# Kernel optimization log

Hardware: AMD Instinct MI355X
Metric: run time of the kernel (lower is better)

## Reference

```python
import jax, jax.numpy as jnp
import numpy as np

N_NODES = 100000
N_EDGES = 1600000
D_IN = 128
D_OUT = 128
EPS = 1e-5


def setup_inputs() -> dict:
    key = jax.random.key(0)
    ks = jax.random.split(key, 5)
    x = jax.random.normal(ks[0], (N_NODES, D_IN), dtype=jnp.float32)
    edge_index = jax.random.randint(ks[1], (2, N_EDGES), 0, N_NODES, dtype=jnp.int64)
    scale = 1.0 / np.sqrt(D_IN)
    W_root = jax.random.normal(ks[2], (D_IN, D_OUT), dtype=jnp.float32) * scale
    W_rel = jax.random.normal(ks[3], (D_IN, D_OUT), dtype=jnp.float32) * scale
    b_rel = jax.random.normal(ks[4], (D_OUT,), dtype=jnp.float32) * 0.01
    gamma = jnp.ones((D_OUT,), dtype=jnp.float32)
    beta = jnp.zeros((D_OUT,), dtype=jnp.float32)
    return {"x": x, "edge_index": edge_index, "W_root": W_root, "W_rel": W_rel,
            "b_rel": b_rel, "gamma": gamma, "beta": beta}


def reference(x, edge_index, W_root, W_rel, b_rel, gamma, beta):
    # GraphConv: out = aggr(x_j) @ W_rel + b_rel + x @ W_root   (aggr = sum)
    src = edge_index[0]
    dst = edge_index[1]
    aggr = jax.ops.segment_sum(x[src], dst, num_segments=x.shape[0])  # [N, D_IN]
    h = aggr @ W_rel + b_rel + x @ W_root                              # [N, D_OUT]
    # NodeLevelBatchNorm (training mode: batch stats over node dim, biased var)
    mean = jnp.mean(h, axis=0)
    var = jnp.mean(jnp.square(h - mean), axis=0)
    h_norm = (h - mean) * jax.lax.rsqrt(var + EPS) * gamma + beta
    return jax.nn.relu(h_norm)
```

## Files before the change

kernel.cpp:

```cpp
#include <hip/hip_runtime.h>

#define N_NODES 100000
#define N_EDGES 1600000
#define D 128
#define NB 196
#define EPT 10
#define CHUNK 2560
#define BIN_BLOCKS 625
#define CVT_X_BLOCKS 6250
#define ZROW N_NODES
#define PBK 13312

typedef __bf16 bf16x8 __attribute__((ext_vector_type(8)));
typedef float f32x4 __attribute__((ext_vector_type(4)));

__device__ __forceinline__ unsigned f2bf(float f) {
    unsigned u = __float_as_uint(f);
    return (u + 0x7fffu + ((u >> 16) & 1u)) >> 16;
}
__device__ __forceinline__ float bf_lo(unsigned u) { return __uint_as_float(u << 16); }
__device__ __forceinline__ float bf_hi(unsigned u) { return __uint_as_float(u & 0xffff0000u); }

__global__ __launch_bounds__(256) void prep_kernel(const float* __restrict__ x,
                                                   const float* __restrict__ Wrel,
                                                   const float* __restrict__ Wroot,
                                                   const int* __restrict__ ei,
                                                   unsigned short* __restrict__ x_bf,
                                                   unsigned short* __restrict__ Wt,
                                                   int* __restrict__ bcount) {
    __shared__ int h[256];
    int b = blockIdx.x;
    int t = threadIdx.x;
    if (b < CVT_X_BLOCKS) {
        size_t i = ((size_t)b * 256 + t) * 8;
        float4 v0 = *(const float4*)(x + i);
        float4 v1 = *(const float4*)(x + i + 4);
        uint4 p;
        p.x = f2bf(v0.x) | (f2bf(v0.y) << 16);
        p.y = f2bf(v0.z) | (f2bf(v0.w) << 16);
        p.z = f2bf(v1.x) | (f2bf(v1.y) << 16);
        p.w = f2bf(v1.z) | (f2bf(v1.w) << 16);
        *(uint4*)(x_bf + i) = p;
    } else if (b < CVT_X_BLOCKS + 128) {
        int c = b - CVT_X_BLOCKS;
        float v = (t < 128) ? Wrel[t * D + c] : Wroot[(t - 128) * D + c];
        Wt[c * 256 + t] = (unsigned short)f2bf(v);
    } else if (b == CVT_X_BLOCKS + 128) {
        if (t < 16) *(uint4*)(x_bf + (size_t)ZROW * D + t * 8) = make_uint4(0, 0, 0, 0);
    } else {
        int blk = b - (CVT_X_BLOCKS + 129);
        h[t] = 0;
        __syncthreads();
        int base = blk * CHUNK;
#pragma unroll
        for (int i = 0; i < EPT; ++i) {
            int dst = ei[N_EDGES + base + i * 256 + t];
            atomicAdd(&h[dst >> 9], 1);
        }
        __syncthreads();
        if (t < NB && h[t]) atomicAdd(&bcount[t], h[t]);
    }
}

__global__ __launch_bounds__(256) void bscan_kernel(const int* __restrict__ bcount,
                                                    int* __restrict__ bucket_base,
                                                    int* __restrict__ bcur) {
    __shared__ int s[256];
    int t = threadIdx.x;
    int v = (t < NB) ? bcount[t] : 0;
    s[t] = v;
    __syncthreads();
    for (int off = 1; off < 256; off <<= 1) {
        int a = (t >= off) ? s[t - off] : 0;
        __syncthreads();
        s[t] += a;
        __syncthreads();
    }
    int excl = s[t] - v;
    if (t < NB) {
        bucket_base[t] = excl;
        bcur[t] = excl;
    }
    if (t == NB) bucket_base[NB] = N_EDGES;
}

__global__ __launch_bounds__(256) void binify_kernel(const int* __restrict__ ei,
                                                     int* __restrict__ bcur,
                                                     unsigned* __restrict__ epk) {
    __shared__ int lhist[256];
    __shared__ int lstart[256];
    __shared__ int lfill[256];
    __shared__ int gbase[256];
    __shared__ uint2 stage[CHUNK];

    int t = threadIdx.x;
    int base = blockIdx.x * CHUNK;
    lhist[t] = 0;
    lfill[t] = 0;
    __syncthreads();

    int src[EPT], dst[EPT];
#pragma unroll
    for (int i = 0; i < EPT; ++i) {
        int e = base + i * 256 + t;
        src[i] = ei[e];
        dst[i] = ei[N_EDGES + e];
        atomicAdd(&lhist[dst[i] >> 9], 1);
    }
    __syncthreads();

    int v = lhist[t];
    lstart[t] = v;
    __syncthreads();
    for (int off = 1; off < 256; off <<= 1) {
        int a = (t >= off) ? lstart[t - off] : 0;
        __syncthreads();
        lstart[t] += a;
        __syncthreads();
    }
    int excl = lstart[t] - v;
    if (t < NB && v > 0) gbase[t] = atomicAdd(&bcur[t], v);
    __syncthreads();
    lstart[t] = excl;
    __syncthreads();

#pragma unroll
    for (int i = 0; i < EPT; ++i) {
        int b = dst[i] >> 9;
        int lp = atomicAdd(&lfill[b], 1);
        stage[lstart[b] + lp] = make_uint2((unsigned)src[i], (unsigned)dst[i]);
    }
    __syncthreads();

    for (int i = t; i < CHUNK; i += 256) {
        uint2 p = stage[i];
        int b = (int)(p.y >> 9);
        unsigned code = p.x | ((p.y & 511u) << 17);
        epk[gbase[b] + (i - lstart[b])] = code;
    }
}

__global__ __launch_bounds__(256) void place_kernel(const unsigned* __restrict__ epk,
                                                    const int* __restrict__ bucket_base,
                                                    int* __restrict__ rbeg,
                                                    int* __restrict__ rend,
                                                    int* __restrict__ srcs) {
    __shared__ int cnt[512];
    __shared__ int sA[512];
    __shared__ int sB[512];
    __shared__ int cursor[512];
    int b = blockIdx.x;
    int t = threadIdx.x;
    int pbeg = bucket_base[b];
    int pend = bucket_base[b + 1];
    int R = b * PBK;

    cnt[t] = 0;
    cnt[t + 256] = 0;
    __syncthreads();
    for (int i = pbeg + t; i < pend; i += 256)
        atomicAdd(&cnt[epk[i] >> 17], 1);
    __syncthreads();

    for (int j = t; j < 512; j += 256) sA[j] = j ? ((cnt[j - 1] + 7) & ~7) : 0;
    __syncthreads();
    int* cur = sA;
    int* nxt = sB;
    for (int off = 1; off < 512; off <<= 1) {
        for (int j = t; j < 512; j += 256)
            nxt[j] = cur[j] + ((j >= off) ? cur[j - off] : 0);
        __syncthreads();
        int* tm = cur; cur = nxt; nxt = tm;
    }

    for (int j = t; j < 512; j += 256) {
        int pj = (cnt[j] + 7) & ~7;
        int s = R + cur[j];
        int g = (b << 9) + j;
        if (g < 100352) { rbeg[g] = s; rend[g] = s + pj; }
        cursor[j] = s;
    }
    __syncthreads();

    for (int i = pbeg + t; i < pend; i += 256) {
        unsigned code = epk[i];
        int pos = atomicAdd(&cursor[code >> 17], 1);
        srcs[pos] = (int)(code & 0x1FFFFu);
    }
    __syncthreads();

    for (int j = t; j < 512; j += 256) {
        int endp = R + cur[j] + ((cnt[j] + 7) & ~7);
        for (int p = cursor[j]; p < endp; ++p) srcs[p] = ZROW;
    }
}

__global__ __launch_bounds__(256) void gather_kernel(const unsigned short* __restrict__ x_bf,
                                                     const int* __restrict__ rbeg,
                                                     const int* __restrict__ rend,
                                                     const int* __restrict__ srcs,
                                                     unsigned short* __restrict__ aggr_bf) {
    int t = threadIdx.x;
    int node = blockIdx.x * 16 + (t >> 4);
    int l16 = t & 15;
    int e = rbeg[node];
    int end = rend[node];
    const unsigned short* xp = x_bf + l16 * 8;
    float a0 = 0.f, a1 = 0.f, a2 = 0.f, a3 = 0.f;
    float a4 = 0.f, a5 = 0.f, a6 = 0.f, a7 = 0.f;
    for (; e + 15 < end; e += 16) {
        int4 s0 = *(const int4*)(srcs + e);
        int4 s1 = *(const int4*)(srcs + e + 4);
        int4 s2 = *(const int4*)(srcs + e + 8);
        int4 s3 = *(const int4*)(srcs + e + 12);
        uint4 u[16];
        u[0]  = *(const uint4*)(xp + (size_t)s0.x * D);
        u[1]  = *(const uint4*)(xp + (size_t)s0.y * D);
        u[2]  = *(const uint4*)(xp + (size_t)s0.z * D);
        u[3]  = *(const uint4*)(xp + (size_t)s0.w * D);
        u[4]  = *(const uint4*)(xp + (size_t)s1.x * D);
        u[5]  = *(const uint4*)(xp + (size_t)s1.y * D);
        u[6]  = *(const uint4*)(xp + (size_t)s1.z * D);
        u[7]  = *(const uint4*)(xp + (size_t)s1.w * D);
        u[8]  = *(const uint4*)(xp + (size_t)s2.x * D);
        u[9]  = *(const uint4*)(xp + (size_t)s2.y * D);
        u[10] = *(const uint4*)(xp + (size_t)s2.z * D);
        u[11] = *(const uint4*)(xp + (size_t)s2.w * D);
        u[12] = *(const uint4*)(xp + (size_t)s3.x * D);
        u[13] = *(const uint4*)(xp + (size_t)s3.y * D);
        u[14] = *(const uint4*)(xp + (size_t)s3.z * D);
        u[15] = *(const uint4*)(xp + (size_t)s3.w * D);
#pragma unroll
        for (int i = 0; i < 16; ++i) {
            a0 += bf_lo(u[i].x);
            a1 += bf_hi(u[i].x);
            a2 += bf_lo(u[i].y);
            a3 += bf_hi(u[i].y);
            a4 += bf_lo(u[i].z);
            a5 += bf_hi(u[i].z);
            a6 += bf_lo(u[i].w);
            a7 += bf_hi(u[i].w);
        }
    }
    if (e < end) {
        int4 s0 = *(const int4*)(srcs + e);
        int4 s1 = *(const int4*)(srcs + e + 4);
        uint4 u[8];
        u[0] = *(const uint4*)(xp + (size_t)s0.x * D);
        u[1] = *(const uint4*)(xp + (size_t)s0.y * D);
        u[2] = *(const uint4*)(xp + (size_t)s0.z * D);
        u[3] = *(const uint4*)(xp + (size_t)s0.w * D);
        u[4] = *(const uint4*)(xp + (size_t)s1.x * D);
        u[5] = *(const uint4*)(xp + (size_t)s1.y * D);
        u[6] = *(const uint4*)(xp + (size_t)s1.z * D);
        u[7] = *(const uint4*)(xp + (size_t)s1.w * D);
#pragma unroll
        for (int i = 0; i < 8; ++i) {
            a0 += bf_lo(u[i].x);
            a1 += bf_hi(u[i].x);
            a2 += bf_lo(u[i].y);
            a3 += bf_hi(u[i].y);
            a4 += bf_lo(u[i].z);
            a5 += bf_hi(u[i].z);
            a6 += bf_lo(u[i].w);
            a7 += bf_hi(u[i].w);
        }
    }
    uint4 w;
    w.x = f2bf(a0) | (f2bf(a1) << 16);
    w.y = f2bf(a2) | (f2bf(a3) << 16);
    w.z = f2bf(a4) | (f2bf(a5) << 16);
    w.w = f2bf(a6) | (f2bf(a7) << 16);
    *(uint4*)(aggr_bf + (size_t)node * D + l16 * 8) = w;
}

__global__ __launch_bounds__(256) void gemm_mfma(const unsigned short* __restrict__ aggr_bf,
                                                 const unsigned short* __restrict__ x_bf,
                                                 const unsigned short* __restrict__ Wt,
                                                 const float* __restrict__ brel,
                                                 unsigned short* __restrict__ h_bf,
                                                 float* __restrict__ gsum,
                                                 float* __restrict__ gss) {
    __shared__ unsigned short Bf[2048 * 8];
    __shared__ float sbias[128];
    __shared__ float SredS[4][128];
    __shared__ float SredQ[4][128];

    const int t = threadIdx.x;
    const int wave = t >> 6;
    const int lane = t & 63;
    const int quad = lane >> 4;
    const int l16 = lane & 15;
    const int blockRow = blockIdx.x * 128;

    if (t < 128) sbias[t] = brel[t];

    f32x4 acc[2][8];
#pragma unroll
    for (int i = 0; i < 2; ++i)
#pragma unroll
        for (int j = 0; j < 8; ++j) acc[i][j] = (f32x4){0.f, 0.f, 0.f, 0.f};

    const int rowb = blockRow + wave * 32;

#pragma unroll
    for (int half = 0; half < 2; ++half) {
#pragma unroll
        for (int f = t; f < 2048; f += 256) {
            int kcl = f >> 9;
            int ct = (f >> 6) & 7;
            int ln = f & 63;
            int col = ct * 16 + (ln & 15);
            int kb = half * 128 + kcl * 32 + ((ln >> 4) << 3);
            *(uint4*)&Bf[f * 8] = *(const uint4*)(Wt + col * 256 + kb);
        }
        __syncthreads();

        const unsigned short* Asrc = half ? x_bf : aggr_bf;
#pragma unroll
        for (int kcl = 0; kcl < 4; ++kcl) {
            const int k0 = kcl * 32 + quad * 8;
            bf16x8 af0 = *(const bf16x8*)(Asrc + (size_t)(rowb + l16) * D + k0);
            bf16x8 af1 = *(const bf16x8*)(Asrc + (size_t)(rowb + 16 + l16) * D + k0);
#pragma unroll
            for (int ct = 0; ct < 8; ++ct) {
                bf16x8 bfrag = *(const bf16x8*)&Bf[((kcl * 8 + ct) * 64 + lane) * 8];
                acc[0][ct] = __builtin_amdgcn_mfma_f32_16x16x32_bf16(af0, bfrag, acc[0][ct], 0, 0, 0);
                acc[1][ct] = __builtin_amdgcn_mfma_f32_16x16x32_bf16(af1, bfrag, acc[1][ct], 0, 0, 0);
            }
        }
        if (half == 0) __syncthreads();
    }

    float csum[8], css[8];
#pragma unroll
    for (int ct = 0; ct < 8; ++ct) { csum[ct] = 0.f; css[ct] = 0.f; }

#pragma unroll
    for (int rt = 0; rt < 2; ++rt) {
#pragma unroll
        for (int ct = 0; ct < 8; ++ct) {
            int col = ct * 16 + l16;
            float bv = sbias[col];
#pragma unroll
            for (int reg = 0; reg < 4; ++reg) {
                int row = blockRow + wave * 32 + rt * 16 + quad * 4 + reg;
                if (row < N_NODES) {
                    float v = acc[rt][ct][reg] + bv;
                    h_bf[(size_t)row * D + col] = (unsigned short)f2bf(v);
                    csum[ct] += v;
                    css[ct] += v * v;
                }
            }
        }
    }
#pragma unroll
    for (int ct = 0; ct < 8; ++ct) {
        float s = csum[ct], q = css[ct];
        s += __shfl_xor(s, 16);
        s += __shfl_xor(s, 32);
        q += __shfl_xor(q, 16);
        q += __shfl_xor(q, 32);
        if (quad == 0) {
            SredS[wave][ct * 16 + l16] = s;
            SredQ[wave][ct * 16 + l16] = q;
        }
    }
    __syncthreads();
    if (t < 128) {
        float s = SredS[0][t] + SredS[1][t] + SredS[2][t] + SredS[3][t];
        float q = SredQ[0][t] + SredQ[1][t] + SredQ[2][t] + SredQ[3][t];
        unsafeAtomicAdd(&gsum[t], s);
        unsafeAtomicAdd(&gss[t], q);
    }
}

__global__ __launch_bounds__(256) void norm_kernel(const unsigned short* __restrict__ h_bf,
                                                   float* __restrict__ out,
                                                   const float* __restrict__ gsum,
                                                   const float* __restrict__ gss,
                                                   const float* __restrict__ gamma,
                                                   const float* __restrict__ beta) {
    __shared__ float sscale[128];
    __shared__ float sshift[128];
    int t = threadIdx.x;
    if (t < 128) {
        const float inv_n = 1.0f / (float)N_NODES;
        float mean = gsum[t] * inv_n;
        float var = gss[t] * inv_n - mean * mean;
        float rs = rsqrtf(var + 1e-5f);
        float sc = gamma[t] * rs;
        sscale[t] = sc;
        sshift[t] = beta[t] - mean * sc;
    }
    __syncthreads();
    size_t e = ((size_t)blockIdx.x * 256 + t) * 4;
    if (e >= (size_t)N_NODES * D) return;
    int c = (int)(e & 127);
    uint2 u = *(const uint2*)(h_bf + e);
    float4 v;
    v.x = fmaxf(bf_lo(u.x) * sscale[c + 0] + sshift[c + 0], 0.f);
    v.y = fmaxf(bf_hi(u.x) * sscale[c + 1] + sshift[c + 1], 0.f);
    v.z = fmaxf(bf_lo(u.y) * sscale[c + 2] + sshift[c + 2], 0.f);
    v.w = fmaxf(bf_hi(u.y) * sscale[c + 3] + sshift[c + 3], 0.f);
    *(float4*)(out + e) = v;
}

extern "C" void kernel_launch(void* const* d_in, const int* in_sizes, int n_in,
                              void* d_out, int out_size, void* d_ws, size_t ws_size,
                              hipStream_t stream) {
    const float* x     = (const float*)d_in[0];
    const int*   ei    = (const int*)d_in[1];
    const float* Wroot = (const float*)d_in[2];
    const float* Wrel  = (const float*)d_in[3];
    const float* brel  = (const float*)d_in[4];
    const float* gamma = (const float*)d_in[5];
    const float* beta  = (const float*)d_in[6];
    float* out = (float*)d_out;

    unsigned short* aggr_bf = (unsigned short*)d_ws;
    unsigned short* x_bf    = aggr_bf + (size_t)N_NODES * D;
    unsigned short* Wt      = x_bf + (size_t)(N_NODES + 1) * D;
    float* gsum  = (float*)(Wt + 128 * 256);
    float* gss   = gsum + 128;
    int* bcount  = (int*)(gss + 128);
    int* bucket_base = bcount + 256;
    int* bcur    = bucket_base + 256;
    int* rbeg    = bcur + 256;
    int* rend    = rbeg + 100352;
    unsigned* epk = (unsigned*)(rend + 100352);
    int* srcs    = (int*)(epk + N_EDGES);
    unsigned short* h_bf = (unsigned short*)epk;

    hipMemsetAsync(gsum, 0, 512 * sizeof(int), stream);

    prep_kernel<<<CVT_X_BLOCKS + 129 + BIN_BLOCKS, 256, 0, stream>>>(
        x, Wrel, Wroot, ei, x_bf, Wt, bcount);
    bscan_kernel<<<1, 256, 0, stream>>>(bcount, bucket_base, bcur);
    binify_kernel<<<BIN_BLOCKS, 256, 0, stream>>>(ei, bcur, epk);
    place_kernel<<<NB, 256, 0, stream>>>(epk, bucket_base, rbeg, rend, srcs);
    gather_kernel<<<N_NODES / 16, 256, 0, stream>>>(x_bf, rbeg, rend, srcs, aggr_bf);
    gemm_mfma<<<(N_NODES + 127) / 128, 256, 0, stream>>>(aggr_bf, x_bf, Wt, brel, h_bf, gsum, gss);
    norm_kernel<<<12500, 256, 0, stream>>>(h_bf, out, gsum, gss, gamma, beta);
}
```

Before: 287.7 us.

## Fuse neighbor gather into MFMA GEMM via shared-memory A tile

Replaces the separate gather kernel and GEMM with one kernel. Each block gathers aggregated features for its 128 rows directly into an LDS tile laid out in MFMA fragment order, then runs both GEMM halves. This removes the global write and re-read of the bf16 aggregate buffer and one launch. In exchange, LDS use per block doubles, which lowers occupancy for the latency-bound gather, and the gather loop has fewer loads in flight per thread.

```diff
diff --git a/kernel.cpp b/kernel.cpp
--- a/kernel.cpp
+++ b/kernel.cpp
@@ -195,92 +195,16 @@
     }
 }
 
-__global__ __launch_bounds__(256) void gather_kernel(const unsigned short* __restrict__ x_bf,
-                                                     const int* __restrict__ rbeg,
-                                                     const int* __restrict__ rend,
-                                                     const int* __restrict__ srcs,
-                                                     unsigned short* __restrict__ aggr_bf) {
-    int t = threadIdx.x;
-    int node = blockIdx.x * 16 + (t >> 4);
-    int l16 = t & 15;
-    int e = rbeg[node];
-    int end = rend[node];
-    const unsigned short* xp = x_bf + l16 * 8;
-    float a0 = 0.f, a1 = 0.f, a2 = 0.f, a3 = 0.f;
-    float a4 = 0.f, a5 = 0.f, a6 = 0.f, a7 = 0.f;
-    for (; e + 15 < end; e += 16) {
-        int4 s0 = *(const int4*)(srcs + e);
-        int4 s1 = *(const int4*)(srcs + e + 4);
-        int4 s2 = *(const int4*)(srcs + e + 8);
-        int4 s3 = *(const int4*)(srcs + e + 12);
-        uint4 u[16];
-        u[0]  = *(const uint4*)(xp + (size_t)s0.x * D);
-        u[1]  = *(const uint4*)(xp + (size_t)s0.y * D);
-        u[2]  = *(const uint4*)(xp + (size_t)s0.z * D);
-        u[3]  = *(const uint4*)(xp + (size_t)s0.w * D);
-        u[4]  = *(const uint4*)(xp + (size_t)s1.x * D);
-        u[5]  = *(const uint4*)(xp + (size_t)s1.y * D);
-        u[6]  = *(const uint4*)(xp + (size_t)s1.z * D);
-        u[7]  = *(const uint4*)(xp + (size_t)s1.w * D);
-        u[8]  = *(const uint4*)(xp + (size_t)s2.x * D);
-        u[9]  = *(const uint4*)(xp + (size_t)s2.y * D);
-        u[10] = *(const uint4*)(xp + (size_t)s2.z * D);
-        u[11] = *(const uint4*)(xp + (size_t)s2.w * D);
-        u[12] = *(const uint4*)(xp + (size_t)s3.x * D);
-        u[13] = *(const uint4*)(xp + (size_t)s3.y * D);
-        u[14] = *(const uint4*)(xp + (size_t)s3.z * D);
-        u[15] = *(const uint4*)(xp + (size_t)s3.w * D);
-#pragma unroll
-        for (int i = 0; i < 16; ++i) {
-            a0 += bf_lo(u[i].x);
-            a1 += bf_hi(u[i].x);
-            a2 += bf_lo(u[i].y);
-            a3 += bf_hi(u[i].y);
-            a4 += bf_lo(u[i].z);
-            a5 += bf_hi(u[i].z);
-            a6 += bf_lo(u[i].w);
-            a7 += bf_hi(u[i].w);
-        }
-    }
-    if (e < end) {
-        int4 s0 = *(const int4*)(srcs + e);
-        int4 s1 = *(const int4*)(srcs + e + 4);
-        uint4 u[8];
-        u[0] = *(const uint4*)(xp + (size_t)s0.x * D);
-        u[1] = *(const uint4*)(xp + (size_t)s0.y * D);
-        u[2] = *(const uint4*)(xp + (size_t)s0.z * D);
-        u[3] = *(const uint4*)(xp + (size_t)s0.w * D);
-        u[4] = *(const uint4*)(xp + (size_t)s1.x * D);
-        u[5] = *(const uint4*)(xp + (size_t)s1.y * D);
-        u[6] = *(const uint4*)(xp + (size_t)s1.z * D);
-        u[7] = *(const uint4*)(xp + (size_t)s1.w * D);
-#pragma unroll
-        for (int i = 0; i < 8; ++i) {
-            a0 += bf_lo(u[i].x);
-            a1 += bf_hi(u[i].x);
-            a2 += bf_lo(u[i].y);
-            a3 += bf_hi(u[i].y);
-            a4 += bf_lo(u[i].z);
-            a5 += bf_hi(u[i].z);
-            a6 += bf_lo(u[i].w);
-            a7 += bf_hi(u[i].w);
-        }
-    }
-    uint4 w;
-    w.x = f2bf(a0) | (f2bf(a1) << 16);
-    w.y = f2bf(a2) | (f2bf(a3) << 16);
-    w.z = f2bf(a4) | (f2bf(a5) << 16);
-    w.w = f2bf(a6) | (f2bf(a7) << 16);
-    *(uint4*)(aggr_bf + (size_t)node * D + l16 * 8) = w;
-}
-
-__global__ __launch_bounds__(256) void gemm_mfma(const unsigned short* __restrict__ aggr_bf,
-                                                 const unsigned short* __restrict__ x_bf,
-                                                 const unsigned short* __restrict__ Wt,
-                                                 const float* __restrict__ brel,
-                                                 unsigned short* __restrict__ h_bf,
-                                                 float* __restrict__ gsum,
-                                                 float* __restrict__ gss) {
+__global__ __launch_bounds__(256) void fused_gemm(const unsigned short* __restrict__ x_bf,
+                                                  const int* __restrict__ rbeg,
+                                                  const int* __restrict__ rend,
+                                                  const int* __restrict__ srcs,
+                                                  const unsigned short* __restrict__ Wt,
+                                                  const float* __restrict__ brel,
+                                                  unsigned short* __restrict__ h_bf,
+                                                  float* __restrict__ gsum,
+                                                  float* __restrict__ gss) {
+    __shared__ unsigned short Af[2048 * 8];
     __shared__ unsigned short Bf[2048 * 8];
     __shared__ float sbias[128];
     __shared__ float SredS[4][128];
@@ -295,41 +219,107 @@
 
     if (t < 128) sbias[t] = brel[t];
 
+#pragma unroll
+    for (int f = t; f < 2048; f += 256) {
+        int kcl = f >> 9;
+        int ct = (f >> 6) & 7;
+        int ln = f & 63;
+        int col = ct * 16 + (ln & 15);
+        int kb = kcl * 32 + ((ln >> 4) << 3);
+        *(uint4*)&Bf[f * 8] = *(const uint4*)(Wt + col * 256 + kb);
+    }
+
+    const unsigned short* xp = x_bf + l16 * 8;
+#pragma unroll 1
+    for (int g = 0; g < 8; ++g) {
+        int r = wave * 32 + g * 4 + quad;
+        int node = blockRow + r;
+        int e = rbeg[node];
+        int end = rend[node];
+        float a0 = 0.f, a1 = 0.f, a2 = 0.f, a3 = 0.f;
+        float a4 = 0.f, a5 = 0.f, a6 = 0.f, a7 = 0.f;
+        for (; e < end; e += 8) {
+            int4 s0 = *(const int4*)(srcs + e);
+            int4 s1 = *(const int4*)(srcs + e + 4);
+            uint4 u0 = *(const uint4*)(xp + (size_t)s0.x * D);
+            uint4 u1 = *(const uint4*)(xp + (size_t)s0.y * D);
+            uint4 u2 = *(const uint4*)(xp + (size_t)s0.z * D);
+            uint4 u3 = *(const uint4*)(xp + (size_t)s0.w * D);
+            uint4 u4 = *(const uint4*)(xp + (size_t)s1.x * D);
+            uint4 u5 = *(const uint4*)(xp + (size_t)s1.y * D);
+            uint4 u6 = *(const uint4*)(xp + (size_t)s1.z * D);
+            uint4 u7 = *(const uint4*)(xp + (size_t)s1.w * D);
+            a0 += bf_lo(u0.x) + bf_lo(u1.x) + bf_lo(u2.x) + bf_lo(u3.x)
+                + bf_lo(u4.x) + bf_lo(u5.x) + bf_lo(u6.x) + bf_lo(u7.x);
+            a1 += bf_hi(u0.x) + bf_hi(u1.x) + bf_hi(u2.x) + bf_hi(u3.x)
+                + bf_hi(u4.x) + bf_hi(u5.x) + bf_hi(u6.x) + bf_hi(u7.x);
+            a2 += bf_lo(u0.y) + bf_lo(u1.y) + bf_lo(u2.y) + bf_lo(u3.y)
+                + bf_lo(u4.y) + bf_lo(u5.y) + bf_lo(u6.y) + bf_lo(u7.y);
+            a3 += bf_hi(u0.y) + bf_hi(u1.y) + bf_hi(u2.y) + bf_hi(u3.y)
+                + bf_hi(u4.y) + bf_hi(u5.y) + bf_hi(u6.y) + bf_hi(u7.y);
+            a4 += bf_lo(u0.z) + bf_lo(u1.z) + bf_lo(u2.z) + bf_lo(u3.z)
+                + bf_lo(u4.z) + bf_lo(u5.z) + bf_lo(u6.z) + bf_lo(u7.z);
+            a5 += bf_hi(u0.z) + bf_hi(u1.z) + bf_hi(u2.z) + bf_hi(u3.z)
+                + bf_hi(u4.z) + bf_hi(u5.z) + bf_hi(u6.z) + bf_hi(u7.z);
+            a6 += bf_lo(u0.w) + bf_lo(u1.w) + bf_lo(u2.w) + bf_lo(u3.w)
+                + bf_lo(u4.w) + bf_lo(u5.w) + bf_lo(u6.w) + bf_lo(u7.w);
+            a7 += bf_hi(u0.w) + bf_hi(u1.w) + bf_hi(u2.w) + bf_hi(u3.w)
+                + bf_hi(u4.w) + bf_hi(u5.w) + bf_hi(u6.w) + bf_hi(u7.w);
+        }
+        uint4 w;
+        w.x = f2bf(a0) | (f2bf(a1) << 16);
+        w.y = f2bf(a2) | (f2bf(a3) << 16);
+        w.z = f2bf(a4) | (f2bf(a5) << 16);
+        w.w = f2bf(a6) | (f2bf(a7) << 16);
+        int c = l16;
+        int wf = ((r >> 5) << 3) + (((r >> 4) & 1) << 2) + (c >> 2);
+        int L = ((c & 3) << 4) + (r & 15);
+        *(uint4*)&Af[(wf * 64 + L) * 8] = w;
+    }
+    __syncthreads();
+
     f32x4 acc[2][8];
 #pragma unroll
     for (int i = 0; i < 2; ++i)
 #pragma unroll
         for (int j = 0; j < 8; ++j) acc[i][j] = (f32x4){0.f, 0.f, 0.f, 0.f};
 
+#pragma unroll
+    for (int kcl = 0; kcl < 4; ++kcl) {
+        bf16x8 af0 = *(const bf16x8*)&Af[(((wave << 3) + kcl) * 64 + lane) * 8];
+        bf16x8 af1 = *(const bf16x8*)&Af[(((wave << 3) + 4 + kcl) * 64 + lane) * 8];
+#pragma unroll
+        for (int ct = 0; ct < 8; ++ct) {
+            bf16x8 bfrag = *(const bf16x8*)&Bf[((kcl * 8 + ct) * 64 + lane) * 8];
+            acc[0][ct] = __builtin_amdgcn_mfma_f32_16x16x32_bf16(af0, bfrag, acc[0][ct], 0, 0, 0);
+            acc[1][ct] = __builtin_amdgcn_mfma_f32_16x16x32_bf16(af1, bfrag, acc[1][ct], 0, 0, 0);
+        }
+    }
+    __syncthreads();
+
+#pragma unroll
+    for (int f = t; f < 2048; f += 256) {
+        int kcl = f >> 9;
+        int ct = (f >> 6) & 7;
+        int ln = f & 63;
+        int col = ct * 16 + (ln & 15);
+        int kb = 128 + kcl * 32 + ((ln >> 4) << 3);
+        *(uint4*)&Bf[f * 8] = *(const uint4*)(Wt + col * 256 + kb);
+    }
+    __syncthreads();
+
     const int rowb = blockRow + wave * 32;
-
-#pragma unroll
-    for (int half = 0; half < 2; ++half) {
-#pragma unroll
-        for (int f = t; f < 2048; f += 256) {
-            int kcl = f >> 9;
-            int ct = (f >> 6) & 7;
-            int ln = f & 63;
-            int col = ct * 16 + (ln & 15);
-            int kb = half * 128 + kcl * 32 + ((ln >> 4) << 3);
-            *(uint4*)&Bf[f * 8] = *(const uint4*)(Wt + col * 256 + kb);
-        }
-        __syncthreads();
-
-        const unsigned short* Asrc = half ? x_bf : aggr_bf;
-#pragma unroll
-        for (int kcl = 0; kcl < 4; ++kcl) {
-            const int k0 = kcl * 32 + quad * 8;
-            bf16x8 af0 = *(const bf16x8*)(Asrc + (size_t)(rowb + l16) * D + k0);
-            bf16x8 af1 = *(const bf16x8*)(Asrc + (size_t)(rowb + 16 + l16) * D + k0);
-#pragma unroll
-            for (int ct = 0; ct < 8; ++ct) {
-                bf16x8 bfrag = *(const bf16x8*)&Bf[((kcl * 8 + ct) * 64 + lane) * 8];
-                acc[0][ct] = __builtin_amdgcn_mfma_f32_16x16x32_bf16(af0, bfrag, acc[0][ct], 0, 0, 0);
-                acc[1][ct] = __builtin_amdgcn_mfma_f32_16x16x32_bf16(af1, bfrag, acc[1][ct], 0, 0, 0);
-            }
-        }
-        if (half == 0) __syncthreads();
+#pragma unroll
+    for (int kcl = 0; kcl < 4; ++kcl) {
+        const int k0 = kcl * 32 + quad * 8;
+        bf16x8 af0 = *(const bf16x8*)(x_bf + (size_t)(rowb + l16) * D + k0);
+        bf16x8 af1 = *(const bf16x8*)(x_bf + (size_t)(rowb + 16 + l16) * D + k0);
+#pragma unroll
+        for (int ct = 0; ct < 8; ++ct) {
+            bf16x8 bfrag = *(const bf16x8*)&Bf[((kcl * 8 + ct) * 64 + lane) * 8];
+            acc[0][ct] = __builtin_amdgcn_mfma_f32_16x16x32_bf16(af0, bfrag, acc[0][ct], 0, 0, 0);
+            acc[1][ct] = __builtin_amdgcn_mfma_f32_16x16x32_bf16(af1, bfrag, acc[1][ct], 0, 0, 0);
+        }
     }
 
     float csum[8], css[8];
@@ -418,9 +408,9 @@
     const float* beta  = (const float*)d_in[6];
     float* out = (float*)d_out;
 
-    unsigned short* aggr_bf = (unsigned short*)d_ws;
-    unsigned short* x_bf    = aggr_bf + (size_t)N_NODES * D;
-    unsigned short* Wt      = x_bf + (size_t)(N_NODES + 1) * D;
+    unsigned short* h_bf = (unsigned short*)d_ws;
+    unsigned short* x_bf = h_bf + (size_t)N_NODES * D;
+    unsigned short* Wt   = x_bf + (size_t)(N_NODES + 1) * D;
     float* gsum  = (float*)(Wt + 128 * 256);
     float* gss   = gsum + 128;
     int* bcount  = (int*)(gss + 128);
@@ -430,7 +420,6 @@
     int* rend    = rbeg + 100352;
     unsigned* epk = (unsigned*)(rend + 100352);
     int* srcs    = (int*)(epk + N_EDGES);
-    unsigned short* h_bf = (unsigned short*)epk;
 
     hipMemsetAsync(gsum, 0, 512 * sizeof(int), stream);
 
@@ -439,7 +428,7 @@
     bscan_kernel<<<1, 256, 0, stream>>>(bcount, bucket_base, bcur);
     binify_kernel<<<BIN_BLOCKS, 256, 0, stream>>>(ei, bcur, epk);
     place_kernel<<<NB, 256, 0, stream>>>(epk, bucket_base, rbeg, rend, srcs);
-    gather_kernel<<<N_NODES / 16, 256, 0, stream>>>(x_bf, rbeg, rend, srcs, aggr_bf);
-    gemm_mfma<<<(N_NODES + 127) / 128, 256, 0, stream>>>(aggr_bf, x_bf, Wt, brel, h_bf, gsum, gss);
+    fused_gemm<<<(N_NODES + 127) / 128, 256, 0, stream>>>(
+        x_bf, rbeg, rend, srcs, Wt, brel, h_bf, gsum, gss);
     norm_kernel<<<12500, 256, 0, stream>>>(h_bf, out, gsum, gss, gamma, beta);
 }
```

Measured after the change: 276.4 us. 3.9% less time.
